# Kernel tuning notes

Measured on AMD Instinct MI355X. Metric: run time of the kernel, lower is better.

The kernel has to match this reference:

```python
import jax, jax.numpy as jnp
import numpy as np

EOS_ID = 1
E = 512
VS = 50000
VT = 50000
S_LEN = 128
T_LEN = 128


def setup_inputs() -> dict:
    key = jax.random.key(0)
    ks = jax.random.split(key, 16)
    sc = 0.05
    inp = {
        'source_words': jax.random.randint(ks[0], (S_LEN,), 0, VS, dtype=jnp.int64 if jax.config.jax_enable_x64 else jnp.int32),
        'target_words': jax.random.randint(ks[1], (T_LEN,), 0, VT, dtype=jnp.int64 if jax.config.jax_enable_x64 else jnp.int32),
        'W_x_hi': jax.random.normal(ks[2], (VS, E), jnp.float32) * sc,
        'W_y_hi': jax.random.normal(ks[3], (VT, E), jnp.float32) * sc,
        'enc_W_ih': jax.random.normal(ks[4], (4 * E, E), jnp.float32) * sc,
        'enc_W_hh': jax.random.normal(ks[5], (4 * E, E), jnp.float32) * sc,
        'enc_b_ih': jax.random.normal(ks[6], (4 * E,), jnp.float32) * sc,
        'enc_b_hh': jax.random.normal(ks[7], (4 * E,), jnp.float32) * sc,
        'dec_W_ih': jax.random.normal(ks[8], (4 * E, E), jnp.float32) * sc,
        'dec_W_hh': jax.random.normal(ks[9], (4 * E, E), jnp.float32) * sc,
        'dec_b_ih': jax.random.normal(ks[10], (4 * E,), jnp.float32) * sc,
        'dec_b_hh': jax.random.normal(ks[11], (4 * E,), jnp.float32) * sc,
        'W_hr_y': jax.random.normal(ks[12], (VT, E), jnp.float32) * sc,
        'b_hr_y': jax.random.normal(ks[13], (VT,), jnp.float32) * sc,
    }
    return inp


def _lstm_cell(x, h, c, W_ih, W_hh, b_ih, b_hh):
    # torch LSTMCell gate order: input, forget, cell(g), output
    gates = x @ W_ih.T + b_ih + h @ W_hh.T + b_hh  # [4E]
    i, f, g, o = jnp.split(gates, 4)
    c_new = jax.nn.sigmoid(f) * c + jax.nn.sigmoid(i) * jnp.tanh(g)
    h_new = jax.nn.sigmoid(o) * jnp.tanh(c_new)
    return h_new, c_new


def reference(source_words, target_words, W_x_hi, W_y_hi,
              enc_W_ih, enc_W_hh, enc_b_ih, enc_b_hh,
              dec_W_ih, dec_W_hh, dec_b_ih, dec_b_hh,
              W_hr_y, b_hr_y):
    e = W_x_hi.shape[1]
    h0 = jnp.zeros((e,), W_x_hi.dtype)

    # ---- encode: one LSTMCell step per source token ----
    def enc_step(carry, tok):
        h, c = carry
        x = W_x_hi[tok]
        return _lstm_cell(x, h, c, enc_W_ih, enc_W_hh, enc_b_ih, enc_b_hh), None

    (h, _c), _ = jax.lax.scan(enc_step, (h0, h0), source_words)

    # cell state is reset to zeros before decoding (as in the torch code)
    c = jnp.zeros_like(h)

    # ---- decode with teacher forcing; targets = target_words ++ [EOS] ----
    targets = jnp.concatenate([target_words, jnp.array([EOS_ID], target_words.dtype)])
    hi0 = W_x_hi[EOS_ID]  # first decoder input uses the SOURCE embedding of EOS

    def dec_step(carry, tok):
        h, c, hi = carry
        h, c = _lstm_cell(hi, h, c, dec_W_ih, dec_W_hh, dec_b_ih, dec_b_hh)
        logits = W_hr_y @ h + b_hr_y                       # [VT]
        loss = -jax.nn.log_softmax(logits)[tok]            # CE, batch=1 mean
        hi_next = W_y_hi[tok]
        return (h, c, hi_next), loss

    _, losses = jax.lax.scan(dec_step, (h, c, hi0), targets)
    return jnp.sum(losses)
```

## Files before the change

### kernel.cpp

```cpp
#include <hip/hip_runtime.h>
#include <cfloat>
#include <cmath>

#define E      512
#define FOURE  2048
#define VT     50000
#define SLEN   128
#define TLEN   129
#define NSTEPS 257
#define NBL    64
#define NC1    245
#define NGRID  309
#define NINBOX 32
#define NCHUNK 196
#define TPAD   132

#define INBOX_OFF  0
#define GXE_OFF    262144
#define PM_OFF     262144
#define PS_OFF     365632
#define TL_OFF     469120
#define HALL_OFF   786432
#define GXD_OFF    1310720
#define PROG_OFF   2367488

__device__ __forceinline__ float sigf(float x){ return 1.0f/(1.0f+__expf(-x)); }
__device__ __forceinline__ float tanhf_fast(float x){ return 2.f*sigf(2.f*x) - 1.f; }

__global__ __launch_bounds__(256) void gx_kernel(
    const int* __restrict__ src, const int* __restrict__ tgt,
    const float* __restrict__ Wx, const float* __restrict__ Wy,
    const float* __restrict__ encWih, const float* __restrict__ encBih, const float* __restrict__ encBhh,
    const float* __restrict__ decWih, const float* __restrict__ decBih, const float* __restrict__ decBhh,
    float* __restrict__ GxE, float* __restrict__ GxD)
{
  __shared__ float xs[8][E];
  const int tid  = threadIdx.x;
  const int tile = blockIdx.x;
  const bool is_dec = tile >= 16;
  const int t0 = is_dec ? (tile-16)*8 : tile*8;
  const int T  = is_dec ? TLEN : SLEN;

  for (int tt=0; tt<8; ++tt){
    int t = t0+tt;
    if (t < T){
      const float* xrow;
      if (is_dec) xrow = (t==0) ? (Wx + (size_t)1*E) : (Wy + (size_t)tgt[t-1]*E);
      else        xrow = Wx + (size_t)src[t]*E;
      xs[tt][tid]     = xrow[tid];
      xs[tt][tid+256] = xrow[tid+256];
    }
  }
  __syncthreads();

  const int r = blockIdx.y*256 + tid;
  const float* wrow = (is_dec ? decWih : encWih) + (size_t)r*E;
  const float  bias = is_dec ? (decBih[r]+decBhh[r]) : (encBih[r]+encBhh[r]);
  float acc[8];
  #pragma unroll
  for (int i=0;i<8;++i) acc[i]=0.f;

  for (int kc=0; kc<E; kc+=4){
    float4 w = *(const float4*)(wrow+kc);
    #pragma unroll
    for (int tt=0; tt<8; ++tt){
      float4 x = *(const float4*)&xs[tt][kc];
      acc[tt] += w.x*x.x + w.y*x.y + w.z*x.z + w.w*x.w;
    }
  }
  float* Gx = is_dec ? GxD : GxE;
  #pragma unroll
  for (int tt=0; tt<8; ++tt){
    int t = t0+tt;
    if (t < T) Gx[(size_t)t*FOURE + r] = bias + acc[tt];
  }
}

__device__ __forceinline__ void load_weights_s(
    const float* __restrict__ Whh, float* __restrict__ wldsw, int j, int lane)
{
  #pragma unroll
  for (int gg=0; gg<4; ++gg){
    const float* wr = Whh + (size_t)(gg*E + j)*E;
    float4 a = *(const float4*)(wr + 4*lane);
    float4 b = *(const float4*)(wr + 4*lane + 256);
    float* dst = wldsw + (size_t)gg*E + (lane&7)*64 + (lane>>3)*4;
    *(float4*)dst      = a;
    *(float4*)(dst+32) = b;
  }
}

__global__ __launch_bounds__(512, 1) void mega_kernel(
    const float* __restrict__ GxE, const float* __restrict__ GxD,
    const float* __restrict__ encWhh, const float* __restrict__ decWhh,
    unsigned long long* __restrict__ inboxes, unsigned* __restrict__ h_all,
    unsigned* __restrict__ prog,
    const float* __restrict__ W, const float* __restrict__ bvec,
    const int* __restrict__ tgt,
    float* __restrict__ pm, float* __restrict__ ps, float* __restrict__ tl)
{
  __shared__ float smemf[17552];
  const int tid = threadIdx.x;

  if (blockIdx.x < NBL){
    const int lane = tid & 63, wave = tid >> 6, bid = blockIdx.x;
    const int g = lane >> 4, k = lane & 15;
    const int j = bid*8 + wave;
    const int row = g*E + j;
    const int slot  = wave*64 + lane;
    const int pslot = slot + 4*(slot>>5);
    float* wldsw = smemf + wave*2048;
    float* hmir  = smemf + 16384;
    const unsigned long long* myslot = inboxes + (size_t)(bid>>1)*1024 + slot;

    load_weights_s(encWhh, wldsw, j, lane);
    float cst = 0.f;

    for (int s=0; s<NSTEPS; ++s){
      if (s == SLEN){
        load_weights_s(decWhh, wldsw, j, lane);
        cst = 0.f;
      }
      const bool isdec = s >= SLEN;
      const int tloc = isdec ? (s - SLEN) : s;
      float gx = (isdec ? GxD : GxE)[(size_t)tloc*FOURE + row];

      float acc = 0.f;
      if (s > 0){
        const int buf = s & 1;
        unsigned long long hu;
        const unsigned long long* hp = myslot + (size_t)buf*512;
        for (int spin=0; spin<(1<<16); ++spin){
          hu = __hip_atomic_load(hp, __ATOMIC_RELAXED, __HIP_MEMORY_SCOPE_AGENT);
          if (__all((unsigned)(hu>>32) == (unsigned)s)) break;
          __builtin_amdgcn_s_sleep(1);
        }
        hmir[buf*576 + pslot] = __uint_as_float((unsigned)hu);
        __syncthreads();
        if (tid==0) atomicAdd(&prog[s*4], 1u);
        const float* hb = hmir + buf*576 + 36*k;
        #pragma unroll
        for (int i=0;i<8;++i){
          float4 h4 = *(const float4*)(hb + 4*i);
          float4 wv = *(const float4*)&wldsw[(size_t)g*E + i*64 + 4*k];
          acc += wv.x*h4.x + wv.y*h4.y + wv.z*h4.z + wv.w*h4.w;
        }
        acc += __shfl_xor(acc,1); acc += __shfl_xor(acc,2);
        acc += __shfl_xor(acc,4); acc += __shfl_xor(acc,8);
      }

      float gv = acc + gx;
      float x1 = __shfl_xor(gv,16);
      float x2 = __shfl_xor(gv,32);
      float x3 = __shfl_xor(x1,32);
      float gi = (g==0)?gv:(g==1)?x1:(g==2)?x2:x3;
      float gf = (g==0)?x1:(g==1)?gv:(g==2)?x3:x2;
      float gg = (g==0)?x2:(g==1)?x3:(g==2)?gv:x1;
      float go = (g==0)?x3:(g==1)?x2:(g==2)?x1:gv;
      cst = sigf(gf)*cst + sigf(gi)*tanhf_fast(gg);
      float hnew = sigf(go)*tanhf_fast(cst);

      unsigned long long pk = ((unsigned long long)(unsigned)(s+1) << 32)
                            |  (unsigned long long)__float_as_uint(hnew);
      if (lane < NINBOX)
        __hip_atomic_store(inboxes + (size_t)lane*1024 + (size_t)((s+1)&1)*512 + j,
                           pk, __ATOMIC_RELAXED, __HIP_MEMORY_SCOPE_AGENT);
      if (isdec && lane==0)
        __hip_atomic_store(h_all + (size_t)tloc*E + j, __float_as_uint(hnew),
                           __ATOMIC_RELAXED, __HIP_MEMORY_SCOPE_AGENT);
    }
    __syncthreads();
    if (tid==0) atomicAdd(&prog[257*4], 1u);

  } else {
    const int bc   = blockIdx.x - NBL;
    const int ty   = bc / 49;
    const int sub  = tid >> 7;
    const int stid = tid & 127;
    const int chunk = (bc % 49)*4 + sub;
    const int wv   = stid >> 6, lane = tid & 63;
    const int t0   = ty * 32;
    const int nt   = (t0 + 32 <= TLEN) ? 32 : (TLEN - t0);
    float* hst  = smemf;
    float* redm = smemf + 16384;
    float* reds = smemf + 16392;

    const int gate_s = (ty < 4) ? (160 + 32*ty) : 257;
    if (tid == 0){
      for (int spin=0; spin<(1<<22); ++spin){
        if (__hip_atomic_load(&prog[gate_s*4], __ATOMIC_RELAXED, __HIP_MEMORY_SCOPE_AGENT)
            >= (unsigned)NBL) break;
        __builtin_amdgcn_s_sleep(16);
      }
    }
    __syncthreads();

    {
      unsigned long long* hst64 = (unsigned long long*)hst;
      const unsigned long long* hsrc = (const unsigned long long*)(h_all + (size_t)t0*E);
      for (int i=tid; i<nt*(E/2); i+=512)
        hst64[i] = __hip_atomic_load(hsrc+i, __ATOMIC_RELAXED, __HIP_MEMORY_SCOPE_AGENT);
    }
    __syncthreads();

    const int c0 = chunk*256 + stid;
    const int c1 = c0 + 128;
    const bool v0 = c0 < VT, v1 = c1 < VT;
    const float* w0 = W + (size_t)(v0 ? c0 : 0)*E;
    const float* w1 = W + (size_t)(v1 ? c1 : 0)*E;

    float acc0[32], acc1[32];
    #pragma unroll
    for (int i=0;i<32;++i){ acc0[i]=0.f; acc1[i]=0.f; }

    for (int kc=0; kc<E; kc+=4){
      float4 wa = *(const float4*)(w0+kc);
      float4 wb = *(const float4*)(w1+kc);
      #pragma unroll
      for (int tt=0; tt<32; ++tt){
        float4 h4 = *(const float4*)&hst[tt*E + kc];
        acc0[tt] += wa.x*h4.x + wa.y*h4.y + wa.z*h4.z + wa.w*h4.w;
        acc1[tt] += wb.x*h4.x + wb.y*h4.y + wb.z*h4.z + wb.w*h4.w;
      }
    }
    const float b0 = v0 ? bvec[c0] : 0.f;
    const float b1 = v1 ? bvec[c1] : 0.f;

    #pragma unroll
    for (int tt=0; tt<32; ++tt){
      const bool act = tt < nt;
      float x0 = v0 ? acc0[tt]+b0 : -FLT_MAX;
      float x1 = v1 ? acc1[tt]+b1 : -FLT_MAX;
      float mx = fmaxf(x0,x1);
      #pragma unroll
      for (int off=1; off<64; off<<=1) mx = fmaxf(mx, __shfl_xor(mx, off));
      if (lane==0) redm[sub*2+wv] = mx;
      __syncthreads();
      mx = fmaxf(redm[sub*2], redm[sub*2+1]);
      float e = (v0 ? __expf(x0-mx) : 0.f) + (v1 ? __expf(x1-mx) : 0.f);
      #pragma unroll
      for (int off=1; off<64; off<<=1) e += __shfl_xor(e, off);
      if (lane==0) reds[sub*2+wv] = e;
      __syncthreads();
      float ssum = reds[sub*2] + reds[sub*2+1];
      if (act){
        int t = t0 + tt;
        if (stid==0){ pm[(size_t)chunk*TPAD + t] = mx; ps[(size_t)chunk*TPAD + t] = ssum; }
        int tok = (t < SLEN) ? tgt[t] : 1;
        if (v0 && c0==tok) tl[t] = x0;
        if (v1 && c1==tok) tl[t] = x1;
      }
      __syncthreads();
    }
  }
}

__global__ __launch_bounds__(256) void c2_kernel(
    const float* __restrict__ pm, const float* __restrict__ ps, const float* __restrict__ tl,
    float* __restrict__ out)
{
  const int tid = threadIdx.x;
  float loss = 0.f;
  if (tid < TLEN){
    float m = -FLT_MAX, ssum = 0.f;
    for (int ch=0; ch<NCHUNK; ++ch){
      float mc = pm[(size_t)ch*TPAD + tid];
      float sc = ps[(size_t)ch*TPAD + tid];
      float nm = fmaxf(m, mc);
      ssum = ssum*__expf(m-nm) + sc*__expf(mc-nm);
      m = nm;
    }
    loss = (m + __logf(ssum)) - tl[tid];
  }
  __shared__ float red[4];
  #pragma unroll
  for (int off=1; off<64; off<<=1) loss += __shfl_xor(loss, off);
  if ((tid & 63)==0) red[tid>>6] = loss;
  __syncthreads();
  if (tid==0) out[0] = red[0]+red[1]+red[2]+red[3];
}

extern "C" void kernel_launch(void* const* d_in, const int* in_sizes, int n_in,
                              void* d_out, int out_size, void* d_ws, size_t ws_size,
                              hipStream_t stream)
{
  const int*   src    = (const int*)  d_in[0];
  const int*   tgt    = (const int*)  d_in[1];
  const float* Wx     = (const float*)d_in[2];
  const float* Wy     = (const float*)d_in[3];
  const float* encWih = (const float*)d_in[4];
  const float* encWhh = (const float*)d_in[5];
  const float* encBih = (const float*)d_in[6];
  const float* encBhh = (const float*)d_in[7];
  const float* decWih = (const float*)d_in[8];
  const float* decWhh = (const float*)d_in[9];
  const float* decBih = (const float*)d_in[10];
  const float* decBhh = (const float*)d_in[11];
  const float* Whr    = (const float*)d_in[12];
  const float* bhr    = (const float*)d_in[13];

  char* ws = (char*)d_ws;
  unsigned long long* inboxes = (unsigned long long*)(ws + INBOX_OFF);
  float* GxE     = (float*)(ws + GXE_OFF);
  float* GxD     = (float*)(ws + GXD_OFF);
  unsigned* hall = (unsigned*)(ws + HALL_OFF);
  unsigned* prog = (unsigned*)(ws + PROG_OFF);
  float* pm      = (float*)(ws + PM_OFF);
  float* ps      = (float*)(ws + PS_OFF);
  float* tl      = (float*)(ws + TL_OFF);

  hipMemsetAsync(ws + INBOX_OFF, 0, NINBOX*1024*8, stream);
  hipMemsetAsync(ws + PROG_OFF, 0, 258*16, stream);

  dim3 ggrid(33, 8);
  gx_kernel<<<ggrid, 256, 0, stream>>>(src, tgt, Wx, Wy,
      encWih, encBih, encBhh, decWih, decBih, decBhh, GxE, GxD);

  mega_kernel<<<NGRID, 512, 0, stream>>>(GxE, GxD, encWhh, decWhh,
      inboxes, hall, prog, Whr, bhr, tgt, pm, ps, tl);

  c2_kernel<<<1, 256, 0, stream>>>(pm, ps, tl, (float*)d_out);
}
```

Measured before the change: 1.102 ms.

## Split logits K-dimension across waves and shrink vocab chunks to 128 rows

The vocab-projection blocks now give each wave half of the embedding dimension for 64 vocab rows per lane-pair, instead of each wave covering full K for distinct rows. Partial sums are combined through shared memory, and then a single wave does the per-timestep softmax partial reductions with no block-level barriers. The chunk count and grid size double to 392 chunks and 554 blocks, which adds parallelism and removes the per-timestep __syncthreads. The cost is an extra LDS reduction pass, a larger partials buffer for the final combine kernel, and an idle second wave during the reduction.

```diff
diff --git a/kernel.cpp b/kernel.cpp
--- a/kernel.cpp
+++ b/kernel.cpp
@@ -9,17 +9,16 @@
 #define TLEN   129
 #define NSTEPS 257
 #define NBL    64
-#define NC1    245
-#define NGRID  309
+#define NGRID  554
 #define NINBOX 32
-#define NCHUNK 196
+#define NCHUNK 392
 #define TPAD   132
 
 #define INBOX_OFF  0
 #define GXE_OFF    262144
 #define PM_OFF     262144
-#define PS_OFF     365632
-#define TL_OFF     469120
+#define PS_OFF     469120
+#define TL_OFF     676096
 #define HALL_OFF   786432
 #define GXD_OFF    1310720
 #define PROG_OFF   2367488
@@ -174,16 +173,15 @@
 
   } else {
     const int bc   = blockIdx.x - NBL;
-    const int ty   = bc / 49;
+    const int ty   = bc / 98;
     const int sub  = tid >> 7;
     const int stid = tid & 127;
-    const int chunk = (bc % 49)*4 + sub;
-    const int wv   = stid >> 6, lane = tid & 63;
+    const int wv   = stid >> 6;
+    const int lane = tid & 63;
+    const int chunk = (bc % 98)*4 + sub;
     const int t0   = ty * 32;
     const int nt   = (t0 + 32 <= TLEN) ? 32 : (TLEN - t0);
     float* hst  = smemf;
-    float* redm = smemf + 16384;
-    float* reds = smemf + 16392;
 
     const int gate_s = (ty < 4) ? (160 + 32*ty) : 257;
     if (tid == 0){
@@ -203,8 +201,8 @@
     }
     __syncthreads();
 
-    const int c0 = chunk*256 + stid;
-    const int c1 = c0 + 128;
+    const int c0 = chunk*128 + lane;
+    const int c1 = c0 + 64;
     const bool v0 = c0 < VT, v1 = c1 < VT;
     const float* w0 = W + (size_t)(v0 ? c0 : 0)*E;
     const float* w1 = W + (size_t)(v1 ? c1 : 0)*E;
@@ -213,7 +211,8 @@
     #pragma unroll
     for (int i=0;i<32;++i){ acc0[i]=0.f; acc1[i]=0.f; }
 
-    for (int kc=0; kc<E; kc+=4){
+    const int kc0 = wv*256;
+    for (int kc=kc0; kc<kc0+256; kc+=4){
       float4 wa = *(const float4*)(w0+kc);
       float4 wb = *(const float4*)(w1+kc);
       #pragma unroll
@@ -223,34 +222,44 @@
         acc1[tt] += wb.x*h4.x + wb.y*h4.y + wb.z*h4.z + wb.w*h4.w;
       }
     }
-    const float b0 = v0 ? bvec[c0] : 0.f;
-    const float b1 = v1 ? bvec[c1] : 0.f;
-
-    #pragma unroll
-    for (int tt=0; tt<32; ++tt){
-      const bool act = tt < nt;
-      float x0 = v0 ? acc0[tt]+b0 : -FLT_MAX;
-      float x1 = v1 ? acc1[tt]+b1 : -FLT_MAX;
-      float mx = fmaxf(x0,x1);
+
+    __syncthreads();
+    float* ldsR = smemf + sub*4160;
+    if (wv == 1){
       #pragma unroll
-      for (int off=1; off<64; off<<=1) mx = fmaxf(mx, __shfl_xor(mx, off));
-      if (lane==0) redm[sub*2+wv] = mx;
-      __syncthreads();
-      mx = fmaxf(redm[sub*2], redm[sub*2+1]);
-      float e = (v0 ? __expf(x0-mx) : 0.f) + (v1 ? __expf(x1-mx) : 0.f);
+      for (int i=0;i<32;++i){
+        ldsR[lane*65 + i]      = acc0[i];
+        ldsR[lane*65 + 32 + i] = acc1[i];
+      }
+    }
+    __syncthreads();
+    if (wv == 0){
       #pragma unroll
-      for (int off=1; off<64; off<<=1) e += __shfl_xor(e, off);
-      if (lane==0) reds[sub*2+wv] = e;
-      __syncthreads();
-      float ssum = reds[sub*2] + reds[sub*2+1];
-      if (act){
-        int t = t0 + tt;
-        if (stid==0){ pm[(size_t)chunk*TPAD + t] = mx; ps[(size_t)chunk*TPAD + t] = ssum; }
-        int tok = (t < SLEN) ? tgt[t] : 1;
-        if (v0 && c0==tok) tl[t] = x0;
-        if (v1 && c1==tok) tl[t] = x1;
-      }
-      __syncthreads();
+      for (int i=0;i<32;++i){
+        acc0[i] += ldsR[lane*65 + i];
+        acc1[i] += ldsR[lane*65 + 32 + i];
+      }
+      const float b0 = v0 ? bvec[c0] : 0.f;
+      const float b1 = v1 ? bvec[c1] : 0.f;
+
+      #pragma unroll
+      for (int tt=0; tt<32; ++tt){
+        if (tt < nt){
+          float x0 = v0 ? acc0[tt]+b0 : -FLT_MAX;
+          float x1 = v1 ? acc1[tt]+b1 : -FLT_MAX;
+          float mx = fmaxf(x0,x1);
+          #pragma unroll
+          for (int off=1; off<64; off<<=1) mx = fmaxf(mx, __shfl_xor(mx, off));
+          float e = (v0 ? __expf(x0-mx) : 0.f) + (v1 ? __expf(x1-mx) : 0.f);
+          #pragma unroll
+          for (int off=1; off<64; off<<=1) e += __shfl_xor(e, off);
+          int t = t0 + tt;
+          if (lane==0){ pm[(size_t)chunk*TPAD + t] = mx; ps[(size_t)chunk*TPAD + t] = e; }
+          int tok = (t < SLEN) ? tgt[t] : 1;
+          if (v0 && c0==tok) tl[t] = x0;
+          if (v1 && c1==tok) tl[t] = x1;
+        }
+      }
     }
   }
 }
```

Result: faster. 1.058 ms, median of 2 (-4.0%).
